# Kernel tuning notes

Hardware: AMD Instinct MI355X
Metric: run time of the kernel (lower is better)

## Reference

```python
import jax, jax.numpy as jnp
import numpy as np

B, T, I, H = 256, 2048, 1, 64


def setup_inputs() -> dict:
    key = jax.random.key(0)
    k_x, k_wi, k_wh, k_bi, k_bh = jax.random.split(key, 5)
    s = 1.0 / np.sqrt(H)  # PyTorch GRU init: U(-1/sqrt(H), 1/sqrt(H))
    return {
        "x": jax.random.normal(k_x, (B, T, I), dtype=jnp.float32),
        "W_ih": jax.random.uniform(k_wi, (3 * H, I), jnp.float32, -s, s),
        "W_hh": jax.random.uniform(k_wh, (3 * H, H), jnp.float32, -s, s),
        "b_ih": jax.random.uniform(k_bi, (3 * H,), jnp.float32, -s, s),
        "b_hh": jax.random.uniform(k_bh, (3 * H,), jnp.float32, -s, s),
    }


def reference(x, W_ih, W_hh, b_ih, b_hh):
    # x: [B, T, I]. PyTorch nn.GRU gate math (gate order: r, z, n).
    b, t, _ = x.shape
    h_dim = W_hh.shape[1]
    # Precompute all input-side gate projections: [B, T, 3H]
    xg = jnp.einsum('bti,gi->btg', x, W_ih) + b_ih
    xg_t = jnp.swapaxes(xg, 0, 1)  # [T, B, 3H] for scan

    def step(h, xg_step):
        gh = h @ W_hh.T + b_hh  # [B, 3H]
        xr, xz, xn = jnp.split(xg_step, 3, axis=-1)
        hr, hz, hn = jnp.split(gh, 3, axis=-1)
        r = jax.nn.sigmoid(xr + hr)
        z = jax.nn.sigmoid(xz + hz)
        n = jnp.tanh(xn + r * hn)
        h_new = (1.0 - z) * n + z * h
        # forward keeps only the LAST hidden channel per timestep (x[:, :, -1])
        return h_new, h_new[:, -1]

    h0 = jnp.zeros((b, h_dim), x.dtype)
    _, ys = jax.lax.scan(step, h0, xg_t)  # ys: [T, B]
    # final view(B, seq_len * feature_size) with feature_size=1 -> [B, T]
    return jnp.swapaxes(ys, 0, 1)
```

## Files before the change

kernel.cpp:

```cpp
#include <hip/hip_runtime.h>

#define B_ 256
#define T_ 2048
#define H_ 64

typedef float f32x4 __attribute__((ext_vector_type(4)));
typedef _Float16 h16x2 __attribute__((ext_vector_type(2)));

__device__ __forceinline__ float fdot2(h16x2 a, h16x2 b, float c) {
#if __has_builtin(__builtin_amdgcn_fdot2)
    return __builtin_amdgcn_fdot2(a, b, c, false);
#else
    float d;
    asm("v_dot2_f32_f16 %0, %1, %2, %3" : "=v"(d) : "v"(a), "v"(b), "v"(c));
    return d;
#endif
}

__device__ __forceinline__ float fast_sigmoid(float v) {
    float e = __builtin_amdgcn_exp2f(-1.4426950408889634f * v);
    return __builtin_amdgcn_rcpf(1.0f + e);
}
__device__ __forceinline__ float fast_tanh(float v) {
    float e = __builtin_amdgcn_exp2f(2.8853900817779268f * v);
    return fmaf(-2.0f, __builtin_amdgcn_rcpf(1.0f + e), 1.0f);
}
__device__ __forceinline__ float readlane_f(float v, int idx) {
    return __builtin_bit_cast(float,
        __builtin_amdgcn_readlane(__builtin_bit_cast(int, v), idx));
}

__global__ __launch_bounds__(64, 1)
void gru_kernel(const float* __restrict__ x,
                const float* __restrict__ W_ih,
                const float* __restrict__ W_hh,
                const float* __restrict__ b_ih,
                const float* __restrict__ b_hh,
                float* __restrict__ out)
{
    __shared__ __align__(16) _Float16 shh[H_];

    const int lane = threadIdx.x;
    const int b    = blockIdx.x;

    h16x2 wr[32], wz[32], wn[32];
    {
        const f32x4* pr = (const f32x4*)(W_hh + (size_t)lane * H_);
        const f32x4* pz = (const f32x4*)(W_hh + (size_t)(64 + lane) * H_);
        const f32x4* pn = (const f32x4*)(W_hh + (size_t)(128 + lane) * H_);
        #pragma unroll
        for (int q = 0; q < 16; ++q) {
            f32x4 vr = pr[q], vz = pz[q], vn = pn[q];
            wr[2*q]   = h16x2{(_Float16)vr.x, (_Float16)vr.y};
            wr[2*q+1] = h16x2{(_Float16)vr.z, (_Float16)vr.w};
            wz[2*q]   = h16x2{(_Float16)vz.x, (_Float16)vz.y};
            wz[2*q+1] = h16x2{(_Float16)vz.z, (_Float16)vz.w};
            wn[2*q]   = h16x2{(_Float16)vn.x, (_Float16)vn.y};
            wn[2*q+1] = h16x2{(_Float16)vn.z, (_Float16)vn.w};
        }
    }
    #pragma unroll
    for (int i = 0; i < 32; ++i)
        asm volatile("" : "+v"(wr[i]), "+v"(wz[i]), "+v"(wn[i]));

    const float wihr = W_ih[lane];
    const float wihz = W_ih[64 + lane];
    const float wihn = W_ih[128 + lane];
    const float br   = b_ih[lane]      + b_hh[lane];
    const float bz   = b_ih[64 + lane] + b_hh[64 + lane];
    const float bhn  = b_hh[128 + lane];
    const float bin  = b_ih[128 + lane];

    const float* __restrict__ xrow = x + (size_t)b * T_;
    float* __restrict__ orow = out + (size_t)b * T_;

    shh[lane] = (_Float16)0.0f;

    float h_own = 0.0f;
    float oval  = 0.0f;
    float xa = xrow[lane];
    float xb = 0.0f;

    for (int tb = 0; tb < T_ / 64; ++tb) {
        if (tb < T_ / 64 - 1) xb = xrow[(tb + 1) * 64 + lane];

        #pragma unroll 4
        for (int t2 = 0; t2 < 64; ++t2) {
            const float xt  = readlane_f(xa, t2);
            const float xpr = fmaf(xt, wihr, br);
            const float xpz = fmaf(xt, wihz, bz);
            const float xpn = fmaf(xt, wihn, bin);

            h16x2 hh[32];
            const f32x4* hp = (const f32x4*)shh;
            #pragma unroll
            for (int q = 0; q < 8; ++q) {
                union { f32x4 f; h16x2 h[4]; } u;
                u.f = hp[q];
                hh[4*q]   = u.h[0];
                hh[4*q+1] = u.h[1];
                hh[4*q+2] = u.h[2];
                hh[4*q+3] = u.h[3];
            }

            float ar[4] = {0,0,0,0}, az[4] = {0,0,0,0}, an[4] = {0,0,0,0};
            #pragma unroll
            for (int i = 0; i < 32; ++i) {
                const int a = i >> 3;
                ar[a] = fdot2(wr[i], hh[i], ar[a]);
                az[a] = fdot2(wz[i], hh[i], az[a]);
                an[a] = fdot2(wn[i], hh[i], an[a]);
            }
            float sr = (ar[0] + ar[1]) + (ar[2] + ar[3]);
            float sz = (az[0] + az[1]) + (az[2] + az[3]);
            float sn = (an[0] + an[1]) + (an[2] + an[3]);

            float r  = fast_sigmoid(sr + xpr);
            float z  = fast_sigmoid(sz + xpz);
            float n  = fast_tanh(fmaf(r, sn + bhn, xpn));
            float h_new = n + z * (h_own - n);
            h_own = h_new;

            shh[lane] = (_Float16)h_new;

            float h63 = readlane_f(h_new, 63);
            oval = (t2 == lane) ? h63 : oval;
        }

        orow[tb * 64 + lane] = oval;
        xa = xb;
    }
}

extern "C" void kernel_launch(void* const* d_in, const int* in_sizes, int n_in,
                              void* d_out, int out_size, void* d_ws, size_t ws_size,
                              hipStream_t stream) {
    const float* x    = (const float*)d_in[0];
    const float* W_ih = (const float*)d_in[1];
    const float* W_hh = (const float*)d_in[2];
    const float* b_ih = (const float*)d_in[3];
    const float* b_hh = (const float*)d_in[4];
    float* out = (float*)d_out;

    dim3 grid(B_), block(64);
    gru_kernel<<<grid, block, 0, stream>>>(x, W_ih, W_hh, b_ih, b_hh, out);
}
```

Measured before the change: 642.8 us.

## Compute GRU recurrent matvec with MFMA instead of packed fp16 dot products

Replaces the per-lane v_dot2 reduction over the hidden state with MFMA 16x16x32 f16 (or 16x16x16 as a fallback). The hidden vector is broadcast as the A operand and the weights are held in registers as B fragments. Only row 0 of each accumulator tile is consumed, so each lane finishes 4 hidden units and lanes 0-15 write the new state back to LDS. The log2(e) scaling of the sigmoid and tanh inputs is folded into the weights and biases ahead of the loop to save multiplies. The goal is to cut the VALU instruction count per timestep, at the cost of MFMA latency on the serial dependency chain and 15/16 of the MFMA work being wasted on duplicate rows.

```diff
diff --git a/kernel.cpp b/kernel.cpp
--- a/kernel.cpp
+++ b/kernel.cpp
@@ -5,30 +5,22 @@
 #define H_ 64
 
 typedef float f32x4 __attribute__((ext_vector_type(4)));
-typedef _Float16 h16x2 __attribute__((ext_vector_type(2)));
+typedef _Float16 h16x4 __attribute__((ext_vector_type(4)));
+typedef _Float16 h16x8 __attribute__((ext_vector_type(8)));
 
-__device__ __forceinline__ float fdot2(h16x2 a, h16x2 b, float c) {
-#if __has_builtin(__builtin_amdgcn_fdot2)
-    return __builtin_amdgcn_fdot2(a, b, c, false);
+#if __has_builtin(__builtin_amdgcn_mfma_f32_16x16x32_f16)
+#define HAS_K32 1
 #else
-    float d;
-    asm("v_dot2_f32_f16 %0, %1, %2, %3" : "=v"(d) : "v"(a), "v"(b), "v"(c));
-    return d;
+#define HAS_K32 0
 #endif
-}
 
-__device__ __forceinline__ float fast_sigmoid(float v) {
-    float e = __builtin_amdgcn_exp2f(-1.4426950408889634f * v);
-    return __builtin_amdgcn_rcpf(1.0f + e);
-}
-__device__ __forceinline__ float fast_tanh(float v) {
-    float e = __builtin_amdgcn_exp2f(2.8853900817779268f * v);
-    return fmaf(-2.0f, __builtin_amdgcn_rcpf(1.0f + e), 1.0f);
-}
 __device__ __forceinline__ float readlane_f(float v, int idx) {
     return __builtin_bit_cast(float,
         __builtin_amdgcn_readlane(__builtin_bit_cast(int, v), idx));
 }
+
+#define NLOG2E (-1.4426950408889634f)
+#define TLOG2E ( 2.8853900817779268f)
 
 __global__ __launch_bounds__(64, 1)
 void gru_kernel(const float* __restrict__ x,
@@ -41,89 +33,144 @@
     __shared__ __align__(16) _Float16 shh[H_];
 
     const int lane = threadIdx.x;
+    const int ln15 = lane & 15;
+    const int kg   = lane >> 4;
     const int b    = blockIdx.x;
 
-    h16x2 wr[32], wz[32], wn[32];
-    {
-        const f32x4* pr = (const f32x4*)(W_hh + (size_t)lane * H_);
-        const f32x4* pz = (const f32x4*)(W_hh + (size_t)(64 + lane) * H_);
-        const f32x4* pn = (const f32x4*)(W_hh + (size_t)(128 + lane) * H_);
+#if HAS_K32
+    h16x8 wb[3][4][2];
+    #pragma unroll
+    for (int g = 0; g < 3; ++g) {
+        const float s = (g == 2) ? TLOG2E : NLOG2E;
         #pragma unroll
-        for (int q = 0; q < 16; ++q) {
-            f32x4 vr = pr[q], vz = pz[q], vn = pn[q];
-            wr[2*q]   = h16x2{(_Float16)vr.x, (_Float16)vr.y};
-            wr[2*q+1] = h16x2{(_Float16)vr.z, (_Float16)vr.w};
-            wz[2*q]   = h16x2{(_Float16)vz.x, (_Float16)vz.y};
-            wz[2*q+1] = h16x2{(_Float16)vz.z, (_Float16)vz.w};
-            wn[2*q]   = h16x2{(_Float16)vn.x, (_Float16)vn.y};
-            wn[2*q+1] = h16x2{(_Float16)vn.z, (_Float16)vn.w};
+        for (int nt = 0; nt < 4; ++nt) {
+            #pragma unroll
+            for (int kt = 0; kt < 2; ++kt) {
+                const float* p = W_hh + (size_t)(g * 64 + nt * 16 + ln15) * H_
+                               + kt * 32 + 8 * kg;
+                h16x8 v;
+                #pragma unroll
+                for (int j = 0; j < 8; ++j) v[j] = (_Float16)(s * p[j]);
+                wb[g][nt][kt] = v;
+            }
         }
     }
+#else
+    h16x4 wb[3][4][4];
     #pragma unroll
-    for (int i = 0; i < 32; ++i)
-        asm volatile("" : "+v"(wr[i]), "+v"(wz[i]), "+v"(wn[i]));
+    for (int g = 0; g < 3; ++g) {
+        const float s = (g == 2) ? TLOG2E : NLOG2E;
+        #pragma unroll
+        for (int nt = 0; nt < 4; ++nt) {
+            #pragma unroll
+            for (int kt = 0; kt < 4; ++kt) {
+                const float* p = W_hh + (size_t)(g * 64 + nt * 16 + ln15) * H_
+                               + kt * 16 + 4 * kg;
+                wb[g][nt][kt] = h16x4{(_Float16)(s * p[0]), (_Float16)(s * p[1]),
+                                      (_Float16)(s * p[2]), (_Float16)(s * p[3])};
+            }
+        }
+    }
+#endif
 
-    const float wihr = W_ih[lane];
-    const float wihz = W_ih[64 + lane];
-    const float wihn = W_ih[128 + lane];
-    const float br   = b_ih[lane]      + b_hh[lane];
-    const float bz   = b_ih[64 + lane] + b_hh[64 + lane];
-    const float bhn  = b_hh[128 + lane];
-    const float bin  = b_ih[128 + lane];
+    float xwr[4], xbr[4], xwz[4], xbz[4], xwn[4], xbn[4], bhn[4];
+    #pragma unroll
+    for (int s = 0; s < 4; ++s) {
+        const int c = 16 * s + ln15;
+        xwr[s] = NLOG2E * W_ih[c];
+        xbr[s] = NLOG2E * (b_ih[c] + b_hh[c]);
+        xwz[s] = NLOG2E * W_ih[64 + c];
+        xbz[s] = NLOG2E * (b_ih[64 + c] + b_hh[64 + c]);
+        xwn[s] = TLOG2E * W_ih[128 + c];
+        xbn[s] = TLOG2E * b_ih[128 + c];
+        bhn[s] = TLOG2E * b_hh[128 + c];
+    }
 
     const float* __restrict__ xrow = x + (size_t)b * T_;
     float* __restrict__ orow = out + (size_t)b * T_;
 
     shh[lane] = (_Float16)0.0f;
 
-    float h_own = 0.0f;
+    float ho[4] = {0.f, 0.f, 0.f, 0.f};
     float oval  = 0.0f;
     float xa = xrow[lane];
     float xb = 0.0f;
+    const f32x4 z4 = {0.f, 0.f, 0.f, 0.f};
 
     for (int tb = 0; tb < T_ / 64; ++tb) {
         if (tb < T_ / 64 - 1) xb = xrow[(tb + 1) * 64 + lane];
 
         #pragma unroll 4
         for (int t2 = 0; t2 < 64; ++t2) {
-            const float xt  = readlane_f(xa, t2);
-            const float xpr = fmaf(xt, wihr, br);
-            const float xpz = fmaf(xt, wihz, bz);
-            const float xpn = fmaf(xt, wihn, bin);
-
-            h16x2 hh[32];
-            const f32x4* hp = (const f32x4*)shh;
+            const float xt = readlane_f(xa, t2);
+            float xpr[4], xpz[4], xpn[4];
             #pragma unroll
-            for (int q = 0; q < 8; ++q) {
-                union { f32x4 f; h16x2 h[4]; } u;
-                u.f = hp[q];
-                hh[4*q]   = u.h[0];
-                hh[4*q+1] = u.h[1];
-                hh[4*q+2] = u.h[2];
-                hh[4*q+3] = u.h[3];
+            for (int s = 0; s < 4; ++s) {
+                xpr[s] = fmaf(xt, xwr[s], xbr[s]);
+                xpz[s] = fmaf(xt, xwz[s], xbz[s]);
+                xpn[s] = fmaf(xt, xwn[s], xbn[s]);
             }
 
-            float ar[4] = {0,0,0,0}, az[4] = {0,0,0,0}, an[4] = {0,0,0,0};
+            f32x4 accr[4], accz[4], accn[4];
+#if HAS_K32
+            h16x8 a0 = *(const h16x8*)&shh[8 * kg];
+            h16x8 a1 = *(const h16x8*)&shh[32 + 8 * kg];
             #pragma unroll
-            for (int i = 0; i < 32; ++i) {
-                const int a = i >> 3;
-                ar[a] = fdot2(wr[i], hh[i], ar[a]);
-                az[a] = fdot2(wz[i], hh[i], az[a]);
-                an[a] = fdot2(wn[i], hh[i], an[a]);
+            for (int nt = 0; nt < 4; ++nt) {
+                accr[nt] = __builtin_amdgcn_mfma_f32_16x16x32_f16(a0, wb[0][nt][0], z4, 0, 0, 0);
+                accz[nt] = __builtin_amdgcn_mfma_f32_16x16x32_f16(a0, wb[1][nt][0], z4, 0, 0, 0);
+                accn[nt] = __builtin_amdgcn_mfma_f32_16x16x32_f16(a0, wb[2][nt][0], z4, 0, 0, 0);
             }
-            float sr = (ar[0] + ar[1]) + (ar[2] + ar[3]);
-            float sz = (az[0] + az[1]) + (az[2] + az[3]);
-            float sn = (an[0] + an[1]) + (an[2] + an[3]);
+            #pragma unroll
+            for (int nt = 0; nt < 4; ++nt) {
+                accr[nt] = __builtin_amdgcn_mfma_f32_16x16x32_f16(a1, wb[0][nt][1], accr[nt], 0, 0, 0);
+                accz[nt] = __builtin_amdgcn_mfma_f32_16x16x32_f16(a1, wb[1][nt][1], accz[nt], 0, 0, 0);
+                accn[nt] = __builtin_amdgcn_mfma_f32_16x16x32_f16(a1, wb[2][nt][1], accn[nt], 0, 0, 0);
+            }
+#else
+            h16x4 af[4];
+            #pragma unroll
+            for (int kt = 0; kt < 4; ++kt)
+                af[kt] = *(const h16x4*)&shh[16 * kt + 4 * kg];
+            #pragma unroll
+            for (int nt = 0; nt < 4; ++nt) {
+                accr[nt] = __builtin_amdgcn_mfma_f32_16x16x16f16(af[0], wb[0][nt][0], z4, 0, 0, 0);
+                accz[nt] = __builtin_amdgcn_mfma_f32_16x16x16f16(af[0], wb[1][nt][0], z4, 0, 0, 0);
+                accn[nt] = __builtin_amdgcn_mfma_f32_16x16x16f16(af[0], wb[2][nt][0], z4, 0, 0, 0);
+            }
+            #pragma unroll
+            for (int kt = 1; kt < 4; ++kt) {
+                #pragma unroll
+                for (int nt = 0; nt < 4; ++nt) {
+                    accr[nt] = __builtin_amdgcn_mfma_f32_16x16x16f16(af[kt], wb[0][nt][kt], accr[nt], 0, 0, 0);
+                    accz[nt] = __builtin_amdgcn_mfma_f32_16x16x16f16(af[kt], wb[1][nt][kt], accz[nt], 0, 0, 0);
+                    accn[nt] = __builtin_amdgcn_mfma_f32_16x16x16f16(af[kt], wb[2][nt][kt], accn[nt], 0, 0, 0);
+                }
+            }
+#endif
 
-            float r  = fast_sigmoid(sr + xpr);
-            float z  = fast_sigmoid(sz + xpz);
-            float n  = fast_tanh(fmaf(r, sn + bhn, xpn));
-            float h_new = n + z * (h_own - n);
-            h_own = h_new;
+            float hnew[4];
+            #pragma unroll
+            for (int s = 0; s < 4; ++s) {
+                float r  = __builtin_amdgcn_rcpf(
+                               1.0f + __builtin_amdgcn_exp2f(accr[s][0] + xpr[s]));
+                float zg = __builtin_amdgcn_rcpf(
+                               1.0f + __builtin_amdgcn_exp2f(accz[s][0] + xpz[s]));
+                float pre = fmaf(r, accn[s][0] + bhn[s], xpn[s]);
+                float n  = fmaf(-2.0f, __builtin_amdgcn_rcpf(
+                               1.0f + __builtin_amdgcn_exp2f(pre)), 1.0f);
+                float h  = fmaf(zg, ho[s] - n, n);
+                ho[s]   = h;
+                hnew[s] = h;
+            }
 
-            shh[lane] = (_Float16)h_new;
+            if (lane < 16) {
+                #pragma unroll
+                for (int s = 0; s < 4; ++s)
+                    shh[16 * s + ln15] = (_Float16)hnew[s];
+            }
 
-            float h63 = readlane_f(h_new, 63);
+            float h63 = readlane_f(hnew[3], 15);
             oval = (t2 == lane) ? h63 : oval;
         }
 
```

Result: slower. 807.8 us (+25.7%).
